# Performance work log

Hardware: AMD Instinct MI355X
Metric: run time of the kernel (lower is better)

Reference implementation:

```python
import jax, jax.numpy as jnp
import numpy as np

H = 512  # hidden_size


def setup_inputs() -> dict:
    key = jax.random.key(0)
    ks = jax.random.split(key, 13)
    B, S, E, V = 64, 2048, 512, 32000
    s = 0.05
    return {
        "word_input": jax.random.randint(ks[0], (B,), 0, V),
        "last_hidden": jax.random.normal(ks[1], (1, B, H), jnp.float32),
        "encoder_outputs": jax.random.normal(ks[2], (S, B, H), jnp.float32),
        "emb": jax.random.normal(ks[3], (V, E), jnp.float32) * s,
        "attn_W": jax.random.normal(ks[4], (H, 2 * H), jnp.float32) * s,
        "attn_b": jax.random.normal(ks[5], (H,), jnp.float32) * s,
        "v": jax.random.normal(ks[6], (H,), jnp.float32) * s,
        "W_ih": jax.random.normal(ks[7], (3 * H, H + E), jnp.float32) * s,
        "W_hh": jax.random.normal(ks[8], (3 * H, H), jnp.float32) * s,
        "b_ih": jax.random.normal(ks[9], (3 * H,), jnp.float32) * s,
        "b_hh": jax.random.normal(ks[10], (3 * H,), jnp.float32) * s,
        "out_W": jax.random.normal(ks[11], (V, 2 * H), jnp.float32) * s,
        "out_b": jax.random.normal(ks[12], (V,), jnp.float32) * s,
    }


def reference(word_input, last_hidden, encoder_outputs, emb, attn_W, attn_b, v,
              W_ih, W_hh, b_ih, b_hh, out_W, out_b):
    # word_input: [B] int; last_hidden: [1,B,H]; encoder_outputs: [S,B,H]
    hid = last_hidden[-1]                       # [B,H]
    enc = jnp.transpose(encoder_outputs, (1, 0, 2))  # [B,S,H]

    # Bahdanau 'concat' attention: tanh(W [h;e] + b) . v  (split W to avoid [B,S,2H])
    Wa, We = attn_W[:, :H], attn_W[:, H:]
    energy = jnp.tanh((hid @ Wa.T)[:, None, :] + jnp.einsum('bsh,kh->bsk', enc, We) + attn_b)
    scores = jnp.einsum('bsk,k->bs', energy, v)       # [B,S]
    attn = jax.nn.softmax(scores, axis=1)             # [B,S]
    context = jnp.einsum('bs,bsh->bh', attn, enc)     # [B,H]

    # GRU step (PyTorch gate layout: r, z, n)
    x = jnp.concatenate([emb[word_input], context], axis=1)  # [B,E+H]
    gi = x @ W_ih.T + b_ih
    gh = hid @ W_hh.T + b_hh
    r = jax.nn.sigmoid(gi[:, :H] + gh[:, :H])
    z = jax.nn.sigmoid(gi[:, H:2 * H] + gh[:, H:2 * H])
    n = jnp.tanh(gi[:, 2 * H:] + r * gh[:, 2 * H:])
    h_new = (1.0 - z) * n + z * hid                   # [B,H]

    logits = jnp.concatenate([h_new, context], axis=1) @ out_W.T + out_b
    output = jax.nn.log_softmax(logits, axis=1)       # [B,V]
    return output, h_new[None]                        # hidden: [1,B,H]
```

## Files before the change

### kernel.cpp

```cpp
#include <hip/hip_runtime.h>
#include <hip/hip_bf16.h>
#include <cstdint>
#include <cstddef>

#define HD 512
#define BB 64
#define SS 2048
#define VV 32000
#define MM (SS*BB)
#define NCH 32

typedef __attribute__((ext_vector_type(8))) short bf16x8;
typedef __attribute__((ext_vector_type(4))) float f32x4;

static __device__ __forceinline__ unsigned short f2bf(float f) {
    union { float f; unsigned u; } x; x.f = f;
    unsigned r = x.u + 0x7fffu + ((x.u >> 16) & 1u);
    return (unsigned short)(r >> 16);
}
static __device__ __forceinline__ unsigned pack2(float a, float b) {
    return (unsigned)f2bf(a) | ((unsigned)f2bf(b) << 16);
}
static __device__ __forceinline__ float rcp_fast(float x) {
    float r; asm("v_rcp_f32 %0, %1" : "=v"(r) : "v"(x)); return r;
}
static __device__ __forceinline__ float tanh_fast(float x) {
    float e = __expf(2.f * x);
    return 1.f - 2.f * rcp_fast(e + 1.f);
}
static __device__ __forceinline__ float sigmoid_fast(float x) {
    return 1.f / (1.f + __expf(-x));
}
static __device__ __forceinline__ void gload16(const void* g, void* l) {
    __builtin_amdgcn_global_load_lds(
        (const __attribute__((address_space(1))) void*)g,
        (__attribute__((address_space(3))) void*)l, 16, 0, 0);
}

__global__ void prep_kernel(const float* __restrict__ hid,
                            const float* __restrict__ attn_W,
                            const float* __restrict__ attn_b,
                            float* __restrict__ qc,
                            uint4* __restrict__ WeB4) {
    int i = blockIdx.x * 256 + threadIdx.x;
    int n = i >> 6, b = i & 63;
    const float* hrow = hid + b * HD;
    const float* wrow = attn_W + (size_t)n * (2 * HD);
    float acc = 0.f;
    for (int k = 0; k < HD; k += 4) {
        float4 h4 = *(const float4*)(hrow + k);
        float4 w4 = *(const float4*)(wrow + k);
        acc += h4.x * w4.x + h4.y * w4.y + h4.z * w4.z + h4.w * w4.w;
    }
    qc[b * HD + n] = acc + attn_b[n];
    int col = (i << 3) & 511;
    int cc0 = col >> 3;
    const float* src = attn_W + (size_t)n * (2 * HD) + HD + col;
    float4 f0 = *(const float4*)(src);
    float4 f1 = *(const float4*)(src + 4);
    uint4 p;
    p.x = pack2(f0.x, f0.y); p.y = pack2(f0.z, f0.w);
    p.z = pack2(f1.x, f1.y); p.w = pack2(f1.z, f1.w);
    int ccs = (cc0 & ~7) | ((cc0 & 7) ^ (n & 7));
    WeB4[n * 64 + ccs] = p;
}

__global__ __launch_bounds__(512, 2) void fattn_kernel(
    const float* __restrict__ enc,
    const uint4* __restrict__ WeB4,
    const float* __restrict__ qc,
    const float* __restrict__ vvec,
    float* __restrict__ oP,
    float* __restrict__ lP)
{
    __shared__ char smem[8192 + 65536 + 2048 + 256];
    uint4* Ald = (uint4*)smem;
    uint4* Bld = (uint4*)(smem + 8192);
    float (*red)[8] = (float(*)[8])(smem + 8192 + 65536);
    float* p_lds = (float*)(smem + 8192 + 65536 + 2048);
    float* opart = (float*)(smem + 8192);

    const int tid = threadIdx.x;
    const int wv = tid >> 6, lane = tid & 63, l15 = lane & 15, l4 = lane >> 4;
    const int b = blockIdx.x & 63;
    const int c = blockIdx.x >> 6;
    const int s0 = c * 64;

    f32x4 acc[4][4] = {};

    const int arow = tid >> 3;
    const int ac8 = tid & 7;
    const float* aptr = enc + ((size_t)(s0 + arow) * 64 + b) * HD + ac8 * 8;
    const int aslot = arow * 8 + (ac8 ^ (arow & 7));

    const int brow = wv * 8 + (lane >> 3);
    const uint4* bg = WeB4 + (size_t)brow * 64 + (lane & 7);

    for (int t = 0; t < 8; ++t) {
        __syncthreads();
        float4 a0 = *(const float4*)(aptr + t * 64);
        float4 a1 = *(const float4*)(aptr + t * 64 + 4);
#pragma unroll
        for (int i = 0; i < 8; ++i)
            gload16(bg + (size_t)i * 64 * 64 + t * 8, &Bld[i * 512 + tid]);
        uint4 u;
        u.x = pack2(a0.x, a0.y); u.y = pack2(a0.z, a0.w);
        u.z = pack2(a1.x, a1.y); u.w = pack2(a1.z, a1.w);
        Ald[aslot] = u;
        __syncthreads();

#pragma unroll
        for (int ks = 0; ks < 2; ++ks) {
            const int chunk = ks * 4 + l4;
            bf16x8 af[4], bfr[4];
#pragma unroll
            for (int mi = 0; mi < 4; ++mi) {
                int row = mi * 16 + l15;
                af[mi] = *(const bf16x8*)&Ald[row * 8 + (chunk ^ (row & 7))];
            }
#pragma unroll
            for (int ni = 0; ni < 4; ++ni) {
                int row = wv * 64 + ni * 16 + l15;
                bfr[ni] = *(const bf16x8*)&Bld[row * 8 + (chunk ^ (row & 7))];
            }
#pragma unroll
            for (int mi = 0; mi < 4; ++mi)
#pragma unroll
                for (int ni = 0; ni < 4; ++ni)
                    acc[mi][ni] = __builtin_amdgcn_mfma_f32_16x16x32_bf16(
                        af[mi], bfr[ni], acc[mi][ni], 0, 0, 0);
        }
    }

    float vv[4], qn[4];
#pragma unroll
    for (int ni = 0; ni < 4; ++ni) {
        int n = wv * 64 + ni * 16 + l15;
        vv[ni] = vvec[n];
        qn[ni] = qc[b * HD + n];
    }
#pragma unroll
    for (int mi = 0; mi < 4; ++mi) {
#pragma unroll
        for (int r = 0; r < 4; ++r) {
            const int rowl = mi * 16 + l4 * 4 + r;
            float s = 0.f;
#pragma unroll
            for (int ni = 0; ni < 4; ++ni)
                s += tanh_fast(acc[mi][ni][r] + qn[ni]) * vv[ni];
#pragma unroll
            for (int msk = 8; msk >= 1; msk >>= 1)
                s += __shfl_xor(s, msk);
            if (l15 == 0) red[rowl][wv] = s;
        }
    }
    __syncthreads();
    if (tid < 64) {
        float t = ((red[tid][0] + red[tid][1]) + (red[tid][2] + red[tid][3]))
                + ((red[tid][4] + red[tid][5]) + (red[tid][6] + red[tid][7]));
        float p = __expf(t);
        p_lds[tid] = p;
        float l = p;
#pragma unroll
        for (int msk = 32; msk >= 1; msk >>= 1) l += __shfl_xor(l, msk);
        if (tid == 0) lP[b * NCH + c] = l;
    }
    __syncthreads();

    float o8[8] = {};
    const float* ebase = enc + ((size_t)(s0 + wv * 8) * 64 + b) * HD + lane * 8;
#pragma unroll
    for (int i = 0; i < 8; ++i) {
        float w = p_lds[wv * 8 + i];
        const float* ep = ebase + (size_t)i * 64 * HD;
        float4 e0 = *(const float4*)(ep);
        float4 e1 = *(const float4*)(ep + 4);
        o8[0] += w * e0.x; o8[1] += w * e0.y; o8[2] += w * e0.z; o8[3] += w * e0.w;
        o8[4] += w * e1.x; o8[5] += w * e1.y; o8[6] += w * e1.z; o8[7] += w * e1.w;
    }
    {
        float4* dst = (float4*)&opart[wv * 512 + lane * 8];
        float4 w0 = {o8[0], o8[1], o8[2], o8[3]};
        float4 w1 = {o8[4], o8[5], o8[6], o8[7]};
        dst[0] = w0; dst[1] = w1;
    }
    __syncthreads();
    float o = 0.f;
#pragma unroll
    for (int w = 0; w < 8; ++w) o += opart[w * 512 + tid];
    oP[((size_t)b * NCH + c) * HD + tid] = o;
}

__global__ void combine_kernel(const float* __restrict__ oP,
                               const float* __restrict__ lP,
                               const int* __restrict__ word,
                               const float* __restrict__ emb,
                               float* __restrict__ x,
                               unsigned* __restrict__ y_bf) {
    const int b = blockIdx.x;
    const int tid = threadIdx.x;
    __shared__ float ctx_lds[512];
    float L = 0.f;
#pragma unroll 8
    for (int c = 0; c < NCH; ++c) L += lP[b * NCH + c];
    float o = 0.f;
#pragma unroll 4
    for (int c = 0; c < NCH; ++c)
        o += oP[((size_t)b * NCH + c) * HD + tid];
    float ctx = o / L;
    x[b * 1024 + HD + tid] = ctx;
    ctx_lds[tid] = ctx;
    x[b * 1024 + tid] = emb[(size_t)word[b] * HD + tid];
    __syncthreads();
    if (tid < 256)
        y_bf[b * 512 + 256 + tid] = pack2(ctx_lds[2 * tid], ctx_lds[2 * tid + 1]);
}

__global__ void gates_kernel(const float* __restrict__ x,
                             const float* __restrict__ hid,
                             const float* __restrict__ W_ih,
                             const float* __restrict__ W_hh,
                             const float* __restrict__ b_ih,
                             const float* __restrict__ b_hh,
                             float* __restrict__ gi, float* __restrict__ gh) {
    const int tid = threadIdx.x;
    const int b = tid & 63;
    const int j = blockIdx.x * 4 + (tid >> 6);
    float agi = 0.f, agh = 0.f;
    const float* xr = x + b * 1024;
    const float* wr = W_ih + (size_t)j * 1024;
    for (int k = 0; k < 1024; k += 4) {
        float4 xv = *(const float4*)(xr + k);
        float4 w4 = *(const float4*)(wr + k);
        agi += xv.x * w4.x + xv.y * w4.y + xv.z * w4.z + xv.w * w4.w;
    }
    const float* hr = hid + b * HD;
    const float* wh = W_hh + (size_t)j * HD;
    for (int k = 0; k < HD; k += 4) {
        float4 hv = *(const float4*)(hr + k);
        float4 w4 = *(const float4*)(wh + k);
        agh += hv.x * w4.x + hv.y * w4.y + hv.z * w4.z + hv.w * w4.w;
    }
    gi[b * 1536 + j] = agi + b_ih[j];
    gh[b * 1536 + j] = agh + b_hh[j];
}

__global__ void hnew_kernel(const float* __restrict__ gi,
                            const float* __restrict__ gh,
                            const float* __restrict__ hid,
                            float* __restrict__ out_h,
                            unsigned* __restrict__ y_bf) {
    const int b = blockIdx.x;
    const int h = threadIdx.x * 2;
    float hn[2];
#pragma unroll
    for (int j = 0; j < 2; ++j) {
        int hh = h + j;
        float r = sigmoid_fast(gi[b * 1536 + hh] + gh[b * 1536 + hh]);
        float z = sigmoid_fast(gi[b * 1536 + 512 + hh] + gh[b * 1536 + 512 + hh]);
        float n = tanh_fast(gi[b * 1536 + 1024 + hh] + r * gh[b * 1536 + 1024 + hh]);
        hn[j] = (1.f - z) * n + z * hid[b * HD + hh];
        out_h[b * HD + hh] = hn[j];
    }
    y_bf[b * 512 + (h >> 1)] = pack2(hn[0], hn[1]);
}

__global__ void logits_kernel(
    const unsigned short* __restrict__ y_bf,
    const float* __restrict__ out_W,
    const float* __restrict__ out_b,
    float* __restrict__ logits)
{
    __shared__ uint4 Yld[64 * 8];
    __shared__ uint4 Wld[128 * 8];
    const int tid = threadIdx.x;
    const int wv = tid >> 6, lane = tid & 63, l15 = lane & 15, l4 = lane >> 4;
    const int n0 = blockIdx.x * 128;

    f32x4 acc[4][2] = {};

    const int s1 = tid, s2 = tid + 256;
    const int r1 = s1 >> 3, g1 = (s1 & 7) ^ (r1 & 7);
    const int r2 = s2 >> 3, g2 = (s2 & 7) ^ (r2 & 7);
    const unsigned short* ya1 = y_bf + (size_t)r1 * 1024 + g1 * 8;
    const unsigned short* ya2 = y_bf + (size_t)r2 * 1024 + g2 * 8;

    const int wr = tid >> 3, wc8 = tid & 7;
    const int wsl = wc8 ^ (wr & 7);
    const float* wp0 = out_W + (size_t)(n0 + wr) * 1024 + wc8 * 8;

    float4 pw[2][8];
#pragma unroll
    for (int i = 0; i < 4; ++i) {
        pw[0][i * 2]     = *(const float4*)(wp0 + (size_t)i * 32768);
        pw[0][i * 2 + 1] = *(const float4*)(wp0 + (size_t)i * 32768 + 4);
    }

#pragma unroll
    for (int t = 0; t < 16; ++t) {
        const int cur = t & 1;
        if (t > 0) {
            asm volatile("s_waitcnt lgkmcnt(0)" ::: "memory");
            __builtin_amdgcn_s_barrier();
        }
        gload16(ya1 + t * 64, &Yld[s1]);
        gload16(ya2 + t * 64, &Yld[s2]);
#pragma unroll
        for (int i = 0; i < 4; ++i) {
            uint4 u;
            u.x = pack2(pw[cur][i * 2].x, pw[cur][i * 2].y);
            u.y = pack2(pw[cur][i * 2].z, pw[cur][i * 2].w);
            u.z = pack2(pw[cur][i * 2 + 1].x, pw[cur][i * 2 + 1].y);
            u.w = pack2(pw[cur][i * 2 + 1].z, pw[cur][i * 2 + 1].w);
            Wld[(wr + 32 * i) * 8 + wsl] = u;
        }
        if (t < 15) {
            const int k1 = (t + 1) * 64;
#pragma unroll
            for (int i = 0; i < 4; ++i) {
                pw[cur ^ 1][i * 2]     = *(const float4*)(wp0 + (size_t)i * 32768 + k1);
                pw[cur ^ 1][i * 2 + 1] = *(const float4*)(wp0 + (size_t)i * 32768 + k1 + 4);
            }
            asm volatile("s_waitcnt vmcnt(8) lgkmcnt(0)" ::: "memory");
        } else {
            asm volatile("s_waitcnt vmcnt(0) lgkmcnt(0)" ::: "memory");
        }
        __builtin_amdgcn_sched_barrier(0);
        __builtin_amdgcn_s_barrier();
        __builtin_amdgcn_sched_barrier(0);

#pragma unroll
        for (int ks = 0; ks < 2; ++ks) {
            const int chunk = ks * 4 + l4;
            bf16x8 af[4], bfr[2];
#pragma unroll
            for (int mi = 0; mi < 4; ++mi) {
                int row = mi * 16 + l15;
                af[mi] = *(const bf16x8*)&Yld[row * 8 + (chunk ^ (row & 7))];
            }
#pragma unroll
            for (int ni = 0; ni < 2; ++ni) {
                int row = wv * 32 + ni * 16 + l15;
                bfr[ni] = *(const bf16x8*)&Wld[row * 8 + (chunk ^ (row & 7))];
            }
#pragma unroll
            for (int mi = 0; mi < 4; ++mi)
#pragma unroll
                for (int ni = 0; ni < 2; ++ni)
                    acc[mi][ni] = __builtin_amdgcn_mfma_f32_16x16x32_bf16(
                        af[mi], bfr[ni], acc[mi][ni], 0, 0, 0);
        }
    }
#pragma unroll
    for (int mi = 0; mi < 4; ++mi) {
#pragma unroll
        for (int r = 0; r < 4; ++r) {
            const int b = mi * 16 + l4 * 4 + r;
#pragma unroll
            for (int ni = 0; ni < 2; ++ni) {
                int n = n0 + wv * 32 + ni * 16 + l15;
                logits[(size_t)b * VV + n] = acc[mi][ni][r] + out_b[n];
            }
        }
    }
}

__global__ void lsm_kernel(float* __restrict__ logits) {
    const int b = blockIdx.x;
    const int tid = threadIdx.x;
    __shared__ float sm[1024];
    float* row = logits + (size_t)b * VV;
    float m = -1e30f;
    for (int i = tid; i < VV; i += 1024) m = fmaxf(m, row[i]);
    sm[tid] = m; __syncthreads();
    for (int o = 512; o > 0; o >>= 1) {
        if (tid < o) sm[tid] = fmaxf(sm[tid], sm[tid + o]);
        __syncthreads();
    }
    m = sm[0]; __syncthreads();
    float s = 0.f;
    for (int i = tid; i < VV; i += 1024) s += __expf(row[i] - m);
    sm[tid] = s; __syncthreads();
    for (int o = 512; o > 0; o >>= 1) {
        if (tid < o) sm[tid] += sm[tid + o];
        __syncthreads();
    }
    float lse = m + __logf(sm[0]);
    for (int i = tid; i < VV; i += 1024) row[i] -= lse;
}

extern "C" void kernel_launch(void* const* d_in, const int* in_sizes, int n_in,
                              void* d_out, int out_size, void* d_ws, size_t ws_size,
                              hipStream_t stream) {
    (void)in_sizes; (void)n_in; (void)out_size; (void)ws_size;
    const int*   word   = (const int*)d_in[0];
    const float* hid    = (const float*)d_in[1];
    const float* enc    = (const float*)d_in[2];
    const float* emb    = (const float*)d_in[3];
    const float* attn_W = (const float*)d_in[4];
    const float* attn_b = (const float*)d_in[5];
    const float* v      = (const float*)d_in[6];
    const float* W_ih   = (const float*)d_in[7];
    const float* W_hh   = (const float*)d_in[8];
    const float* b_ih   = (const float*)d_in[9];
    const float* b_hh   = (const float*)d_in[10];
    const float* out_W  = (const float*)d_in[11];
    const float* out_b  = (const float*)d_in[12];

    float* out    = (float*)d_out;
    float* logits = out;
    float* out_h  = out + (size_t)BB * VV;

    char* ws0 = (char*)d_ws;
    size_t off = 0;
    float* qc      = (float*)(ws0 + off);    off += 64 * 512 * 4;
    uint4* WeB4    = (uint4*)(ws0 + off);    off += 512 * 512 * 2;
    float* oP      = (float*)(ws0 + off);    off += (size_t)BB * NCH * HD * 4;
    float* lP      = (float*)(ws0 + off);    off += BB * NCH * 4;
    float* x       = (float*)(ws0 + off);    off += 64 * 1024 * 4;
    unsigned* y_bf = (unsigned*)(ws0 + off); off += 64 * 1024 * 2;
    float* gi      = (float*)(ws0 + off);    off += 64 * 1536 * 4;
    float* gh      = (float*)(ws0 + off);    off += 64 * 1536 * 4;

    prep_kernel<<<128, 256, 0, stream>>>(hid, attn_W, attn_b, qc, WeB4);
    fattn_kernel<<<BB * NCH, 512, 0, stream>>>(enc, WeB4, qc, v, oP, lP);
    combine_kernel<<<BB, 512, 0, stream>>>(oP, lP, word, emb, x, y_bf);
    gates_kernel<<<384, 256, 0, stream>>>(x, hid, W_ih, W_hh, b_ih, b_hh, gi, gh);
    hnew_kernel<<<BB, 256, 0, stream>>>(gi, gh, hid, out_h, y_bf);
    logits_kernel<<<VV / 128, 256, 0, stream>>>((const unsigned short*)y_bf, out_W, out_b, logits);
    lsm_kernel<<<BB, 1024, 0, stream>>>(logits);
}
```

Before: 333.6 us.

## Software-pipeline attention tile loads, halve logits tile, use hardware bf16 pack

```diff
diff --git a/kernel.cpp b/kernel.cpp
--- a/kernel.cpp
+++ b/kernel.cpp
@@ -13,13 +13,10 @@
 typedef __attribute__((ext_vector_type(8))) short bf16x8;
 typedef __attribute__((ext_vector_type(4))) float f32x4;
 
-static __device__ __forceinline__ unsigned short f2bf(float f) {
-    union { float f; unsigned u; } x; x.f = f;
-    unsigned r = x.u + 0x7fffu + ((x.u >> 16) & 1u);
-    return (unsigned short)(r >> 16);
-}
 static __device__ __forceinline__ unsigned pack2(float a, float b) {
-    return (unsigned)f2bf(a) | ((unsigned)f2bf(b) << 16);
+    unsigned r;
+    asm("v_cvt_pk_bf16_f32 %0, %1, %2" : "=v"(r) : "v"(a), "v"(b));
+    return r;
 }
 static __device__ __forceinline__ float rcp_fast(float x) {
     float r; asm("v_rcp_f32 %0, %1" : "=v"(r) : "v"(x)); return r;
@@ -96,19 +93,29 @@
     const int brow = wv * 8 + (lane >> 3);
     const uint4* bg = WeB4 + (size_t)brow * 64 + (lane & 7);
 
+    float4 pa[2][2];
+    pa[0][0] = *(const float4*)(aptr);
+    pa[0][1] = *(const float4*)(aptr + 4);
+#pragma unroll
+    for (int i = 0; i < 8; ++i)
+        gload16(bg + (size_t)i * 4096, &Bld[i * 512 + tid]);
+    pa[1][0] = *(const float4*)(aptr + 64);
+    pa[1][1] = *(const float4*)(aptr + 68);
+    {
+        uint4 u;
+        u.x = pack2(pa[0][0].x, pa[0][0].y);
+        u.y = pack2(pa[0][0].z, pa[0][0].w);
+        u.z = pack2(pa[0][1].x, pa[0][1].y);
+        u.w = pack2(pa[0][1].z, pa[0][1].w);
+        Ald[aslot] = u;
+    }
+    asm volatile("s_waitcnt vmcnt(2) lgkmcnt(0)" ::: "memory");
+    __builtin_amdgcn_s_barrier();
+    __builtin_amdgcn_sched_barrier(0);
+
+#pragma unroll
     for (int t = 0; t < 8; ++t) {
-        __syncthreads();
-        float4 a0 = *(const float4*)(aptr + t * 64);
-        float4 a1 = *(const float4*)(aptr + t * 64 + 4);
-#pragma unroll
-        for (int i = 0; i < 8; ++i)
-            gload16(bg + (size_t)i * 64 * 64 + t * 8, &Bld[i * 512 + tid]);
-        uint4 u;
-        u.x = pack2(a0.x, a0.y); u.y = pack2(a0.z, a0.w);
-        u.z = pack2(a1.x, a1.y); u.w = pack2(a1.z, a1.w);
-        Ald[aslot] = u;
-        __syncthreads();
-
+        const int cur = t & 1;
 #pragma unroll
         for (int ks = 0; ks < 2; ++ks) {
             const int chunk = ks * 4 + l4;
@@ -129,6 +136,30 @@
                 for (int ni = 0; ni < 4; ++ni)
                     acc[mi][ni] = __builtin_amdgcn_mfma_f32_16x16x32_bf16(
                         af[mi], bfr[ni], acc[mi][ni], 0, 0, 0);
+        }
+        asm volatile("s_waitcnt lgkmcnt(0)" ::: "memory");
+        __builtin_amdgcn_s_barrier();
+        __builtin_amdgcn_sched_barrier(0);
+
+        if (t < 7) {
+#pragma unroll
+            for (int i = 0; i < 8; ++i)
+                gload16(bg + (size_t)i * 4096 + (t + 1) * 8, &Bld[i * 512 + tid]);
+            uint4 u;
+            u.x = pack2(pa[cur ^ 1][0].x, pa[cur ^ 1][0].y);
+            u.y = pack2(pa[cur ^ 1][0].z, pa[cur ^ 1][0].w);
+            u.z = pack2(pa[cur ^ 1][1].x, pa[cur ^ 1][1].y);
+            u.w = pack2(pa[cur ^ 1][1].z, pa[cur ^ 1][1].w);
+            Ald[aslot] = u;
+            if (t < 6) {
+                pa[cur][0] = *(const float4*)(aptr + (t + 2) * 64);
+                pa[cur][1] = *(const float4*)(aptr + (t + 2) * 64 + 4);
+                asm volatile("s_waitcnt vmcnt(2) lgkmcnt(0)" ::: "memory");
+            } else {
+                asm volatile("s_waitcnt vmcnt(0) lgkmcnt(0)" ::: "memory");
+            }
+            __builtin_amdgcn_s_barrier();
+            __builtin_amdgcn_sched_barrier(0);
         }
     }
 
@@ -265,19 +296,19 @@
     y_bf[b * 512 + (h >> 1)] = pack2(hn[0], hn[1]);
 }
 
-__global__ void logits_kernel(
+__global__ __launch_bounds__(256, 4) void logits_kernel(
     const unsigned short* __restrict__ y_bf,
     const float* __restrict__ out_W,
     const float* __restrict__ out_b,
     float* __restrict__ logits)
 {
     __shared__ uint4 Yld[64 * 8];
-    __shared__ uint4 Wld[128 * 8];
+    __shared__ uint4 Wld[64 * 8];
     const int tid = threadIdx.x;
     const int wv = tid >> 6, lane = tid & 63, l15 = lane & 15, l4 = lane >> 4;
-    const int n0 = blockIdx.x * 128;
-
-    f32x4 acc[4][2] = {};
+    const int n0 = blockIdx.x * 64;
+
+    f32x4 acc[4] = {};
 
     const int s1 = tid, s2 = tid + 256;
     const int r1 = s1 >> 3, g1 = (s1 & 7) ^ (r1 & 7);
@@ -288,13 +319,13 @@
     const int wr = tid >> 3, wc8 = tid & 7;
     const int wsl = wc8 ^ (wr & 7);
     const float* wp0 = out_W + (size_t)(n0 + wr) * 1024 + wc8 * 8;
-
-    float4 pw[2][8];
-#pragma unroll
-    for (int i = 0; i < 4; ++i) {
-        pw[0][i * 2]     = *(const float4*)(wp0 + (size_t)i * 32768);
-        pw[0][i * 2 + 1] = *(const float4*)(wp0 + (size_t)i * 32768 + 4);
-    }
+    const float* wp1 = out_W + (size_t)(n0 + wr + 32) * 1024 + wc8 * 8;
+
+    float4 pw[2][4];
+    pw[0][0] = *(const float4*)(wp0);
+    pw[0][1] = *(const float4*)(wp0 + 4);
+    pw[0][2] = *(const float4*)(wp1);
+    pw[0][3] = *(const float4*)(wp1 + 4);
 
 #pragma unroll
     for (int t = 0; t < 16; ++t) {
@@ -302,53 +333,53 @@
         if (t > 0) {
             asm volatile("s_waitcnt lgkmcnt(0)" ::: "memory");
             __builtin_amdgcn_s_barrier();
+            __builtin_amdgcn_sched_barrier(0);
         }
         gload16(ya1 + t * 64, &Yld[s1]);
         gload16(ya2 + t * 64, &Yld[s2]);
-#pragma unroll
-        for (int i = 0; i < 4; ++i) {
+        {
             uint4 u;
-            u.x = pack2(pw[cur][i * 2].x, pw[cur][i * 2].y);
-            u.y = pack2(pw[cur][i * 2].z, pw[cur][i * 2].w);
-            u.z = pack2(pw[cur][i * 2 + 1].x, pw[cur][i * 2 + 1].y);
-            u.w = pack2(pw[cur][i * 2 + 1].z, pw[cur][i * 2 + 1].w);
-            Wld[(wr + 32 * i) * 8 + wsl] = u;
+            u.x = pack2(pw[cur][0].x, pw[cur][0].y);
+            u.y = pack2(pw[cur][0].z, pw[cur][0].w);
+            u.z = pack2(pw[cur][1].x, pw[cur][1].y);
+            u.w = pack2(pw[cur][1].z, pw[cur][1].w);
+            Wld[wr * 8 + wsl] = u;
+            u.x = pack2(pw[cur][2].x, pw[cur][2].y);
+            u.y = pack2(pw[cur][2].z, pw[cur][2].w);
+            u.z = pack2(pw[cur][3].x, pw[cur][3].y);
+            u.w = pack2(pw[cur][3].z, pw[cur][3].w);
+            Wld[(wr + 32) * 8 + wsl] = u;
         }
         if (t < 15) {
             const int k1 = (t + 1) * 64;
-#pragma unroll
-            for (int i = 0; i < 4; ++i) {
-                pw[cur ^ 1][i * 2]     = *(const float4*)(wp0 + (size_t)i * 32768 + k1);
-                pw[cur ^ 1][i * 2 + 1] = *(const float4*)(wp0 + (size_t)i * 32768 + k1 + 4);
-            }
-            asm volatile("s_waitcnt vmcnt(8) lgkmcnt(0)" ::: "memory");
+            pw[cur ^ 1][0] = *(const float4*)(wp0 + k1);
+            pw[cur ^ 1][1] = *(const float4*)(wp0 + k1 + 4);
+            pw[cur ^ 1][2] = *(const float4*)(wp1 + k1);
+            pw[cur ^ 1][3] = *(const float4*)(wp1 + k1 + 4);
+            asm volatile("s_waitcnt vmcnt(4) lgkmcnt(0)" ::: "memory");
         } else {
             asm volatile("s_waitcnt vmcnt(0) lgkmcnt(0)" ::: "memory");
         }
-        __builtin_amdgcn_sched_barrier(0);
         __builtin_amdgcn_s_barrier();
         __builtin_amdgcn_sched_barrier(0);
 
 #pragma unroll
         for (int ks = 0; ks < 2; ++ks) {
             const int chunk = ks * 4 + l4;
-            bf16x8 af[4], bfr[2];
+            bf16x8 af[4], bfr;
 #pragma unroll
             for (int mi = 0; mi < 4; ++mi) {
                 int row = mi * 16 + l15;
                 af[mi] = *(const bf16x8*)&Yld[row * 8 + (chunk ^ (row & 7))];
             }
-#pragma unroll
-            for (int ni = 0; ni < 2; ++ni) {
-                int row = wv * 32 + ni * 16 + l15;
-                bfr[ni] = *(const bf16x8*)&Wld[row * 8 + (chunk ^ (row & 7))];
+            {
+                int row = wv * 16 + l15;
+                bfr = *(const bf16x8*)&Wld[row * 8 + (chunk ^ (row & 7))];
             }
 #pragma unroll
             for (int mi = 0; mi < 4; ++mi)
-#pragma unroll
-                for (int ni = 0; ni < 2; ++ni)
-                    acc[mi][ni] = __builtin_amdgcn_mfma_f32_16x16x32_bf16(
-                        af[mi], bfr[ni], acc[mi][ni], 0, 0, 0);
+                acc[mi] = __builtin_amdgcn_mfma_f32_16x16x32_bf16(
+                    af[mi], bfr, acc[mi], 0, 0, 0);
         }
     }
 #pragma unroll
@@ -356,11 +387,8 @@
 #pragma unroll
         for (int r = 0; r < 4; ++r) {
             const int b = mi * 16 + l4 * 4 + r;
-#pragma unroll
-            for (int ni = 0; ni < 2; ++ni) {
-                int n = n0 + wv * 32 + ni * 16 + l15;
-                logits[(size_t)b * VV + n] = acc[mi][ni][r] + out_b[n];
-            }
+            int n = n0 + wv * 16 + l15;
+            logits[(size_t)b * VV + n] = acc[mi][r] + out_b[n];
         }
     }
 }
@@ -427,6 +455,6 @@
     combine_kernel<<<BB, 512, 0, stream>>>(oP, lP, word, emb, x, y_bf);
     gates_kernel<<<384, 256, 0, stream>>>(x, hid, W_ih, W_hh, b_ih, b_hh, gi, gh);
     hnew_kernel<<<BB, 256, 0, stream>>>(gi, gh, hid, out_h, y_bf);
-    logits_kernel<<<VV / 128, 256, 0, stream>>>((const unsigned short*)y_bf, out_W, out_b, logits);
+    logits_kernel<<<VV / 64, 256, 0, stream>>>((const unsigned short*)y_bf, out_W, out_b, logits);
     lsm_kernel<<<BB, 1024, 0, stream>>>(logits);
 }
```

New measurement: 328.2 us. No clear change (-1.6%).
